# Kernel optimization log

Hardware: AMD Instinct MI355X
Metric: run time of the kernel (lower is better)

Reference implementation:

```python
import jax, jax.numpy as jnp
import numpy as np

N = 100000      # nodes
E = 1600000     # edges
G = 256         # graphs
NF = 2          # dataset.num_features
NC = 2          # dataset.num_classes
DIM = 32
BN_EPS = 1e-5


def _gin_layer(h, src, dst, w_in, b_in, w_out, b_out, gamma, beta):
    # GINConv (eps=0): h' = MLP(h + sum_{j in N(i)} h_j)
    agg = jax.ops.segment_sum(h[src], dst, num_segments=N)  # [N, d] scatter-add
    z = h + agg
    z = jax.nn.relu(z @ w_in + b_in) @ w_out + b_out        # 2-layer MLP
    z = jax.nn.relu(z)
    # BatchNorm1d (training-mode batch stats, biased var as in torch)
    mean = jnp.mean(z, axis=0)
    var = jnp.var(z, axis=0)
    return gamma * (z - mean) * jax.lax.rsqrt(var + BN_EPS) + beta


def setup_inputs() -> dict:
    key = jax.random.key(0)
    ks = jax.random.split(key, 20)
    s = 0.1
    x = jax.random.normal(ks[0], (N, NF), dtype=jnp.float32)
    edge_index = jax.random.randint(ks[1], (2, E), 0, N, dtype=jnp.int64)
    batch = jnp.sort(jax.random.randint(ks[2], (N,), 0, G, dtype=jnp.int64))
    return {
        "x": x,
        "edge_index": edge_index,
        "batch": batch,
        "w1_in": jax.random.normal(ks[3], (NF, DIM), dtype=jnp.float32) * s,
        "b1_in": jnp.zeros((DIM,), jnp.float32),
        "w1_out": jax.random.normal(ks[4], (DIM, DIM), dtype=jnp.float32) * s,
        "b1_out": jnp.zeros((DIM,), jnp.float32),
        "ws_in": jax.random.normal(ks[5], (4, DIM, DIM), dtype=jnp.float32) * s,
        "bs_in": jnp.zeros((4, DIM), jnp.float32),
        "ws_out": jax.random.normal(ks[6], (4, DIM, DIM), dtype=jnp.float32) * s,
        "bs_out": jnp.zeros((4, DIM), jnp.float32),
        "bn_gamma": jnp.ones((5, DIM), jnp.float32),
        "bn_beta": jnp.zeros((5, DIM), jnp.float32),
        "fc1_w": jax.random.normal(ks[7], (DIM, DIM), dtype=jnp.float32) * s,
        "fc1_b": jnp.zeros((DIM,), jnp.float32),
        "fc2_w": jax.random.normal(ks[8], (DIM, NC), dtype=jnp.float32) * s,
        "fc2_b": jnp.zeros((NC,), jnp.float32),
    }


def reference(x, edge_index, batch, w1_in, b1_in, w1_out, b1_out,
              ws_in, bs_in, ws_out, bs_out, bn_gamma, bn_beta,
              fc1_w, fc1_b, fc2_w, fc2_b):
    src, dst = edge_index[0], edge_index[1]
    h = _gin_layer(x, src, dst, w1_in, b1_in, w1_out, b1_out, bn_gamma[0], bn_beta[0])
    for i in range(4):  # convs 2..5 (structurally identical)
        h = _gin_layer(h, src, dst, ws_in[i], bs_in[i], ws_out[i], bs_out[i],
                       bn_gamma[i + 1], bn_beta[i + 1])
    g = jax.ops.segment_sum(h, batch, num_segments=G)  # global_add_pool -> [G, DIM]
    g = jax.nn.relu(g @ fc1_w + fc1_b)
    # dropout is identity in eval mode
    g = g @ fc2_w + fc2_b
    return jax.nn.log_softmax(g, axis=-1)
```

## Files before the change

kernel.cpp:

```cpp
#include <hip/hip_runtime.h>
#include <math.h>

#define NN 100000
#define NE 1600000
#define NG 256
#define NPART 200
#define PS 500
#define CAP 9000
#define EPB 2048
#define NBLK ((NE + EPB - 1) / EPB)
#define DEGB 64
static constexpr float BN_EPS = 1e-5f;

__device__ inline float h2f(unsigned short u) {
    _Float16 h; __builtin_memcpy(&h, &u, 2); return (float)h;
}
__device__ inline unsigned short f2h(float f) {
    _Float16 h = (_Float16)f; unsigned short u; __builtin_memcpy(&u, &h, 2); return u;
}
__device__ inline unsigned int pack2(float a, float b) {
    return (unsigned int)f2h(a) | ((unsigned int)f2h(b) << 16);
}

__global__ __launch_bounds__(256) void bucket_k(const int* __restrict__ src,
                                                const int* __restrict__ dst,
                                                int* __restrict__ bcur,
                                                unsigned int* __restrict__ bpk) {
    __shared__ int cnt[NPART];
    __shared__ int base[NPART];
    int t = threadIdx.x;
    for (int i = t; i < NPART; i += 256) cnt[i] = 0;
    __syncthreads();
    int eb = blockIdx.x * EPB + t * 8;
    bool act = eb < NE;
    int myp[8], myr[8];
    unsigned int pk[8];
    if (act) {
        int4 d0 = *reinterpret_cast<const int4*>(dst + eb);
        int4 d1 = *reinterpret_cast<const int4*>(dst + eb + 4);
        int4 s0 = *reinterpret_cast<const int4*>(src + eb);
        int4 s1 = *reinterpret_cast<const int4*>(src + eb + 4);
        int dd[8] = {d0.x,d0.y,d0.z,d0.w,d1.x,d1.y,d1.z,d1.w};
        int ss[8] = {s0.x,s0.y,s0.z,s0.w,s1.x,s1.y,s1.z,s1.w};
        #pragma unroll
        for (int i = 0; i < 8; i++) {
            int p = dd[i] / PS;
            myp[i] = p;
            pk[i] = ((unsigned int)ss[i] << 9) | (unsigned int)(dd[i] - p * PS);
            myr[i] = atomicAdd(&cnt[p], 1);
        }
    }
    __syncthreads();
    for (int i = t; i < NPART; i += 256)
        base[i] = cnt[i] ? atomicAdd(&bcur[i], cnt[i]) : 0;
    __syncthreads();
    if (act) {
        #pragma unroll
        for (int i = 0; i < 8; i++)
            bpk[myp[i] * CAP + base[myp[i]] + myr[i]] = pk[i];
    }
}

__global__ __launch_bounds__(256) void build_k(const int* __restrict__ bcur,
                                               const unsigned int* __restrict__ bpk,
                                               int* __restrict__ rowptr,
                                               int* __restrict__ csr,
                                               int* __restrict__ perm) {
    __shared__ int hist[PS];
    __shared__ int allc[NPART];
    __shared__ int psum[256];
    __shared__ int bc[DEGB];
    int p = blockIdx.x, t = threadIdx.x;
    int lo = p * PS;
    if (t < NPART) allc[t] = bcur[t];
    for (int i = t; i < PS; i += 256) hist[i] = 0;
    if (t < DEGB) bc[t] = 0;
    __syncthreads();
    int base = 0;
    for (int q = 0; q < p; q++) base += allc[q];
    int cnt = allc[p];
    const unsigned int* bp = bpk + p * CAP;
    const uint4* bp4 = reinterpret_cast<const uint4*>(bp);
    int n4 = cnt >> 2;
    for (int i = t; i < n4; i += 256) {
        uint4 v = bp4[i];
        atomicAdd(&hist[v.x & 511u], 1);
        atomicAdd(&hist[v.y & 511u], 1);
        atomicAdd(&hist[v.z & 511u], 1);
        atomicAdd(&hist[v.w & 511u], 1);
    }
    for (int i = 4 * n4 + t; i < cnt; i += 256) atomicAdd(&hist[bp[i] & 511u], 1);
    __syncthreads();
    int j0 = t * 2;
    int d0v = 0, d1v = 0, tsum = 0;
    if (j0 < PS) {
        d0v = hist[j0]; d1v = hist[j0 + 1];
        tsum = d0v + d1v;
        atomicAdd(&bc[d0v < DEGB ? d0v : DEGB - 1], 1);
        atomicAdd(&bc[d1v < DEGB ? d1v : DEGB - 1], 1);
    }
    psum[t] = tsum;
    __syncthreads();
    for (int off = 1; off < 256; off <<= 1) {
        int v = (t >= off) ? psum[t - off] : 0;
        __syncthreads();
        psum[t] += v;
        __syncthreads();
    }
    int texcl = psum[t] - tsum;
    if (j0 < PS) {
        int run = base + texcl;
        hist[j0] = run; rowptr[lo + j0] = run; run += d0v;
        hist[j0 + 1] = run; rowptr[lo + j0 + 1] = run; run += d1v;
    }
    if (p == NPART - 1 && t == 0) rowptr[NN] = base + cnt;
    __syncthreads();
    if (t == 0) {
        int run = 0;
        #pragma unroll
        for (int b = 0; b < DEGB; b++) { int c = bc[b]; bc[b] = run; run += c; }
    }
    __syncthreads();
    if (j0 < PS) {
        int r0 = atomicAdd(&bc[d0v < DEGB ? d0v : DEGB - 1], 1);
        perm[(PS - 1 - r0) * NPART + p] = lo + j0;
        int r1 = atomicAdd(&bc[d1v < DEGB ? d1v : DEGB - 1], 1);
        perm[(PS - 1 - r1) * NPART + p] = lo + j0 + 1;
    }
    __syncthreads();
    for (int i = t; i < n4; i += 256) {
        uint4 v = bp4[i];
        csr[atomicAdd(&hist[v.x & 511u], 1)] = v.x >> 9;
        csr[atomicAdd(&hist[v.y & 511u], 1)] = v.y >> 9;
        csr[atomicAdd(&hist[v.z & 511u], 1)] = v.z >> 9;
        csr[atomicAdd(&hist[v.w & 511u], 1)] = v.w >> 9;
    }
    for (int i = 4 * n4 + t; i < cnt; i += 256)
        csr[atomicAdd(&hist[bp[i] & 511u], 1)] = bp[i] >> 9;
}

__global__ __launch_bounds__(128) void gmlp1_k(
        const float* __restrict__ x, const int* __restrict__ perm,
        const int* __restrict__ rowptr, const int* __restrict__ csr,
        const float* __restrict__ w_in, const float* __restrict__ b_in,
        const float* __restrict__ w_out, const float* __restrict__ b_out,
        unsigned short* __restrict__ zout, float* __restrict__ stats) {
    __shared__ float lwi[64], lbi[32], lwo[1024], lbo[32];
    __shared__ float zin[64][33];
    int t = threadIdx.x;
    int n = t >> 1, q = t & 1, c0 = q * 16;
    for (int i = t; i < 1024; i += 128) lwo[i] = w_out[i];
    if (t < 64) lwi[t] = w_in[t];
    if (t < 32) { lbi[t] = b_in[t]; lbo[t] = b_out[t]; }
    __syncthreads();
    int gid = blockIdx.x * 64 + n;
    bool act = gid < NN;
    int node = act ? perm[gid] : 0;
    float h0 = 0.f, h1 = 0.f;
    if (act) {
        int rs = rowptr[node], re = rowptr[node + 1];
        if (q == 0) {
            float2 self = *reinterpret_cast<const float2*>(x + 2 * (size_t)node);
            h0 = self.x; h1 = self.y;
        }
        float g0 = 0.f, g1 = 0.f;
        int k = rs + q;
        for (; k + 6 < re; k += 8) {
            int s0 = csr[k], s1 = csr[k + 2], s2 = csr[k + 4], s3 = csr[k + 6];
            float2 v0 = *reinterpret_cast<const float2*>(x + 2 * (size_t)s0);
            float2 v1 = *reinterpret_cast<const float2*>(x + 2 * (size_t)s1);
            float2 v2 = *reinterpret_cast<const float2*>(x + 2 * (size_t)s2);
            float2 v3 = *reinterpret_cast<const float2*>(x + 2 * (size_t)s3);
            h0 += v0.x + v2.x; h1 += v0.y + v2.y;
            g0 += v1.x + v3.x; g1 += v1.y + v3.y;
        }
        for (; k < re; k += 2) {
            int s = csr[k];
            float2 v = *reinterpret_cast<const float2*>(x + 2 * (size_t)s);
            h0 += v.x; h1 += v.y;
        }
        h0 += g0; h1 += g1;
    }
    h0 += __shfl_xor(h0, 1);
    h1 += __shfl_xor(h1, 1);
    float y[16];
    #pragma unroll
    for (int j = 0; j < 16; j++) {
        float a = lbi[c0 + j] + h0 * lwi[c0 + j] + h1 * lwi[32 + c0 + j];
        y[j] = a > 0.f ? a : 0.f;
    }
    #pragma unroll
    for (int j = 0; j < 16; j++) zin[n][c0 + j] = act ? y[j] : 0.f;
    __syncthreads();
    float o[16];
    #pragma unroll
    for (int j = 0; j < 16; j++) o[j] = lbo[c0 + j];
    #pragma unroll
    for (int c = 0; c < 32; c++) {
        float yv = zin[n][c];
        #pragma unroll
        for (int j = 0; j < 16; j++) o[j] += yv * lwo[c * 32 + c0 + j];
    }
    #pragma unroll
    for (int j = 0; j < 16; j++) o[j] = o[j] > 0.f ? o[j] : 0.f;
    if (act) {
        unsigned short* zo = zout + (size_t)node * 32 + c0;
        uint4 wa, wb;
        wa.x = pack2(o[0], o[1]);   wa.y = pack2(o[2], o[3]);
        wa.z = pack2(o[4], o[5]);   wa.w = pack2(o[6], o[7]);
        wb.x = pack2(o[8], o[9]);   wb.y = pack2(o[10], o[11]);
        wb.z = pack2(o[12], o[13]); wb.w = pack2(o[14], o[15]);
        *reinterpret_cast<uint4*>(zo) = wa;
        *reinterpret_cast<uint4*>(zo + 8) = wb;
    }
    __syncthreads();
    #pragma unroll
    for (int j = 0; j < 16; j++) zin[n][c0 + j] = act ? o[j] : 0.f;
    __syncthreads();
    if (t < 32) {
        float s = 0.f, sq = 0.f;
        for (int nn = 0; nn < 64; nn++) {
            float v = zin[nn][t];
            s += v; sq += v * v;
        }
        atomicAdd(&stats[t], s);
        atomicAdd(&stats[32 + t], sq);
    }
}

__global__ __launch_bounds__(128) void gmlp32_k(
        const unsigned short* __restrict__ z, const int* __restrict__ perm,
        const float* __restrict__ statsIn,
        const float* __restrict__ gamma, const float* __restrict__ beta,
        const int* __restrict__ rowptr, const int* __restrict__ csr,
        const float* __restrict__ w_in, const float* __restrict__ b_in,
        const float* __restrict__ w_out, const float* __restrict__ b_out,
        unsigned short* __restrict__ zout, float* __restrict__ statsOut) {
    __shared__ float lwi[1024], lwo[1024], lbi[32], lbo[32], lsc[64];
    __shared__ float zin[64][33];
    int t = threadIdx.x;
    int n = t >> 1, q = t & 1, c0 = q * 16;
    for (int i = t; i < 1024; i += 128) { lwi[i] = w_in[i]; lwo[i] = w_out[i]; }
    if (t < 32) {
        lbi[t] = b_in[t]; lbo[t] = b_out[t];
        float mean = statsIn[t] * (1.f / NN);
        float var  = statsIn[32 + t] * (1.f / NN) - mean * mean;
        float scale = gamma[t] * rsqrtf(var + BN_EPS);
        lsc[t] = scale;
        lsc[32 + t] = beta[t] - mean * scale;
    }
    __syncthreads();
    int gid = blockIdx.x * 64 + n;
    bool act = gid < NN;
    int node = act ? perm[gid] : 0;
    float a[16];
    #pragma unroll
    for (int j = 0; j < 16; j++) a[j] = 0.f;
    float cntf = 0.f;
    if (act) {
        int rs = rowptr[node], re = rowptr[node + 1];
        cntf = (float)(re - rs + 1);
        const unsigned short* zb = z + (size_t)node * 32 + c0;
        uint4 sa = *reinterpret_cast<const uint4*>(zb);
        uint4 sb = *reinterpret_cast<const uint4*>(zb + 8);
        const unsigned short* pa = reinterpret_cast<const unsigned short*>(&sa);
        const unsigned short* pb = reinterpret_cast<const unsigned short*>(&sb);
        #pragma unroll
        for (int j = 0; j < 8; j++) { a[j] = h2f(pa[j]); a[8 + j] = h2f(pb[j]); }
        int k = rs;
        for (; k + 4 <= re; k += 4) {
            int s0 = csr[k], s1 = csr[k + 1], s2 = csr[k + 2], s3 = csr[k + 3];
            const unsigned short* r0 = z + (size_t)s0 * 32 + c0;
            const unsigned short* r1 = z + (size_t)s1 * 32 + c0;
            const unsigned short* r2 = z + (size_t)s2 * 32 + c0;
            const unsigned short* r3 = z + (size_t)s3 * 32 + c0;
            uint4 v0a = *reinterpret_cast<const uint4*>(r0);
            uint4 v0b = *reinterpret_cast<const uint4*>(r0 + 8);
            uint4 v1a = *reinterpret_cast<const uint4*>(r1);
            uint4 v1b = *reinterpret_cast<const uint4*>(r1 + 8);
            uint4 v2a = *reinterpret_cast<const uint4*>(r2);
            uint4 v2b = *reinterpret_cast<const uint4*>(r2 + 8);
            uint4 v3a = *reinterpret_cast<const uint4*>(r3);
            uint4 v3b = *reinterpret_cast<const uint4*>(r3 + 8);
            const unsigned short* q0a = reinterpret_cast<const unsigned short*>(&v0a);
            const unsigned short* q0b = reinterpret_cast<const unsigned short*>(&v0b);
            const unsigned short* q1a = reinterpret_cast<const unsigned short*>(&v1a);
            const unsigned short* q1b = reinterpret_cast<const unsigned short*>(&v1b);
            const unsigned short* q2a = reinterpret_cast<const unsigned short*>(&v2a);
            const unsigned short* q2b = reinterpret_cast<const unsigned short*>(&v2b);
            const unsigned short* q3a = reinterpret_cast<const unsigned short*>(&v3a);
            const unsigned short* q3b = reinterpret_cast<const unsigned short*>(&v3b);
            #pragma unroll
            for (int j = 0; j < 8; j++) {
                a[j]     += (h2f(q0a[j]) + h2f(q1a[j])) + (h2f(q2a[j]) + h2f(q3a[j]));
                a[8 + j] += (h2f(q0b[j]) + h2f(q1b[j])) + (h2f(q2b[j]) + h2f(q3b[j]));
            }
        }
        for (; k < re; k++) {
            int s = csr[k];
            const unsigned short* r = z + (size_t)s * 32 + c0;
            uint4 va = *reinterpret_cast<const uint4*>(r);
            uint4 vb = *reinterpret_cast<const uint4*>(r + 8);
            const unsigned short* qa = reinterpret_cast<const unsigned short*>(&va);
            const unsigned short* qb = reinterpret_cast<const unsigned short*>(&vb);
            #pragma unroll
            for (int j = 0; j < 8; j++) { a[j] += h2f(qa[j]); a[8 + j] += h2f(qb[j]); }
        }
    }
    #pragma unroll
    for (int j = 0; j < 16; j++)
        zin[n][c0 + j] = act ? (a[j] * lsc[c0 + j] + cntf * lsc[32 + c0 + j]) : 0.f;
    __syncthreads();
    float y[16];
    #pragma unroll
    for (int j = 0; j < 16; j++) y[j] = lbi[c0 + j];
    #pragma unroll
    for (int c = 0; c < 32; c++) {
        float zv = zin[n][c];
        #pragma unroll
        for (int j = 0; j < 16; j++) y[j] += zv * lwi[c * 32 + c0 + j];
    }
    #pragma unroll
    for (int j = 0; j < 16; j++) y[j] = y[j] > 0.f ? y[j] : 0.f;
    __syncthreads();
    #pragma unroll
    for (int j = 0; j < 16; j++) zin[n][c0 + j] = y[j];
    __syncthreads();
    float o[16];
    #pragma unroll
    for (int j = 0; j < 16; j++) o[j] = lbo[c0 + j];
    #pragma unroll
    for (int c = 0; c < 32; c++) {
        float yv = zin[n][c];
        #pragma unroll
        for (int j = 0; j < 16; j++) o[j] += yv * lwo[c * 32 + c0 + j];
    }
    #pragma unroll
    for (int j = 0; j < 16; j++) o[j] = o[j] > 0.f ? o[j] : 0.f;
    if (act) {
        unsigned short* zo = zout + (size_t)node * 32 + c0;
        uint4 wa, wb;
        wa.x = pack2(o[0], o[1]);   wa.y = pack2(o[2], o[3]);
        wa.z = pack2(o[4], o[5]);   wa.w = pack2(o[6], o[7]);
        wb.x = pack2(o[8], o[9]);   wb.y = pack2(o[10], o[11]);
        wb.z = pack2(o[12], o[13]); wb.w = pack2(o[14], o[15]);
        *reinterpret_cast<uint4*>(zo) = wa;
        *reinterpret_cast<uint4*>(zo + 8) = wb;
    }
    __syncthreads();
    #pragma unroll
    for (int j = 0; j < 16; j++) zin[n][c0 + j] = act ? o[j] : 0.f;
    __syncthreads();
    if (t < 32) {
        float s = 0.f, sq = 0.f;
        for (int nn = 0; nn < 64; nn++) {
            float v = zin[nn][t];
            s += v; sq += v * v;
        }
        atomicAdd(&statsOut[t], s);
        atomicAdd(&statsOut[32 + t], sq);
    }
}

__global__ __launch_bounds__(256) void pool_seg_k(
        const unsigned short* __restrict__ z,
        const float* __restrict__ statsIn,
        const float* __restrict__ gamma, const float* __restrict__ beta,
        const int* __restrict__ batch, float* __restrict__ g) {
    __shared__ float lsc[64];
    __shared__ float part[32][33];
    int t = threadIdx.x, slot = t >> 3, q = t & 7, c0 = q * 4;
    int gr = blockIdx.x;
    if (t < 32) {
        float mean = statsIn[t] * (1.f / NN);
        float var  = statsIn[32 + t] * (1.f / NN) - mean * mean;
        float scale = gamma[t] * rsqrtf(var + BN_EPS);
        lsc[t] = scale;
        lsc[32 + t] = beta[t] - mean * scale;
    }
    int lo = 0, hi = NN;
    while (lo < hi) { int mid = (lo + hi) >> 1; if (batch[mid] < gr) lo = mid + 1; else hi = mid; }
    int start = lo;
    hi = NN;
    while (lo < hi) { int mid = (lo + hi) >> 1; if (batch[mid] < gr + 1) lo = mid + 1; else hi = mid; }
    int end = lo;
    float a0 = 0.f, a1 = 0.f, a2 = 0.f, a3 = 0.f;
    for (int i = start + slot; i < end; i += 32) {
        ushort4 v = *reinterpret_cast<const ushort4*>(z + (size_t)i * 32 + c0);
        a0 += h2f(v.x); a1 += h2f(v.y); a2 += h2f(v.z); a3 += h2f(v.w);
    }
    part[slot][c0+0] = a0; part[slot][c0+1] = a1;
    part[slot][c0+2] = a2; part[slot][c0+3] = a3;
    __syncthreads();
    if (t < 32) {
        float s = 0.f;
        for (int sl = 0; sl < 32; sl++) s += part[sl][t];
        float cnt = (float)(end - start);
        g[(size_t)gr * 32 + t] = s * lsc[t] + cnt * lsc[32 + t];
    }
}

__global__ __launch_bounds__(256) void head_k(
        const float* __restrict__ g,
        const float* __restrict__ fc1w, const float* __restrict__ fc1b,
        const float* __restrict__ fc2w, const float* __restrict__ fc2b,
        float* __restrict__ out) {
    __shared__ float lw1[1024], lb1[32], lw2[64], lb2[2];
    int t = threadIdx.x;
    for (int i = t; i < 1024; i += 256) lw1[i] = fc1w[i];
    if (t < 32) lb1[t] = fc1b[t];
    if (t < 64) lw2[t] = fc2w[t];
    if (t < 2) lb2[t] = fc2b[t];
    __syncthreads();
    float gv[32];
    #pragma unroll
    for (int c = 0; c < 32; c++) gv[c] = g[(size_t)t * 32 + c];
    float o0 = lb2[0], o1 = lb2[1];
    #pragma unroll 4
    for (int k = 0; k < 32; k++) {
        float a = lb1[k];
        #pragma unroll
        for (int c = 0; c < 32; c++) a += gv[c] * lw1[c * 32 + k];
        a = a > 0.f ? a : 0.f;
        o0 += a * lw2[k * 2 + 0];
        o1 += a * lw2[k * 2 + 1];
    }
    float m = fmaxf(o0, o1);
    float lse = m + logf(expf(o0 - m) + expf(o1 - m));
    out[t * 2 + 0] = o0 - lse;
    out[t * 2 + 1] = o1 - lse;
}

extern "C" void kernel_launch(void* const* d_in, const int* in_sizes, int n_in,
                              void* d_out, int out_size, void* d_ws, size_t ws_size,
                              hipStream_t stream) {
    const float* x      = (const float*)d_in[0];
    const int*   ei     = (const int*)d_in[1];
    const int*   src    = ei;
    const int*   dst    = ei + NE;
    const int*   batch  = (const int*)d_in[2];
    const float* w1_in  = (const float*)d_in[3];
    const float* b1_in  = (const float*)d_in[4];
    const float* w1_out = (const float*)d_in[5];
    const float* b1_out = (const float*)d_in[6];
    const float* ws_in  = (const float*)d_in[7];
    const float* bs_in  = (const float*)d_in[8];
    const float* ws_out = (const float*)d_in[9];
    const float* bs_out = (const float*)d_in[10];
    const float* gamma  = (const float*)d_in[11];
    const float* beta   = (const float*)d_in[12];
    const float* fc1w   = (const float*)d_in[13];
    const float* fc1b   = (const float*)d_in[14];
    const float* fc2w   = (const float*)d_in[15];
    const float* fc2b   = (const float*)d_in[16];
    float* out = (float*)d_out;

    unsigned short* bufA = (unsigned short*)d_ws;
    unsigned short* bufB = bufA + (size_t)NN * 32;
    float* stats  = (float*)(bufB + (size_t)NN * 32);
    int*   bcur   = (int*)(stats + 5 * 64);
    float* g      = (float*)(bcur + NPART);
    int*   perm   = (int*)(g + (size_t)NG * 32);
    int*   rowptr = perm + NN;
    int*   csr    = rowptr + NN + 4;
    unsigned int* bpk = (unsigned int*)(csr + NE);

    hipMemsetAsync(stats, 0, (size_t)(5 * 64 + NPART) * sizeof(int), stream);

    bucket_k<<<NBLK, 256, 0, stream>>>(src, dst, bcur, bpk);
    build_k<<<NPART, 256, 0, stream>>>(bcur, bpk, rowptr, csr, perm);

    gmlp1_k<<<(NN + 63) / 64, 128, 0, stream>>>(x, perm, rowptr, csr,
                                                w1_in, b1_in, w1_out, b1_out, bufA, stats);

    const unsigned short* cur = bufA;
    unsigned short* nxt = bufB;
    for (int j = 0; j < 4; j++) {
        gmlp32_k<<<(NN + 63) / 64, 128, 0, stream>>>(cur, perm, stats + j * 64,
                                              gamma + j * 32, beta + j * 32,
                                              rowptr, csr,
                                              ws_in + j * 1024, bs_in + j * 32,
                                              ws_out + j * 1024, bs_out + j * 32,
                                              nxt, stats + (j + 1) * 64);
        unsigned short* tmp = (unsigned short*)cur; cur = nxt; nxt = tmp;
    }

    pool_seg_k<<<NG, 256, 0, stream>>>(cur, stats + 4 * 64,
                                       gamma + 4 * 32, beta + 4 * 32, batch, g);
    head_k<<<1, 256, 0, stream>>>(g, fc1w, fc1b, fc2w, fc2b, out);
}
```

Measured before the change: 477.4 us.

## Shrink CSR partitions, localize degree-sorted perm, enlarge GIN blocks, unroll gather by 8

Node partitions are halved to 250 nodes (400 partitions), so each build thread handles one node and the packed destination offset uses 8 bits. The degree-sorted permutation is now stored contiguously inside each partition instead of interleaved across partitions, which changes which nodes share a block in the aggregation kernels. The GIN MLP kernel moves to 256-thread blocks of 128 nodes, and its neighbor gather is unrolled by 8 to keep more loads in flight. In exchange it uses more registers and shared memory, and the new perm ordering loses the cross-partition degree balancing.

```diff
diff --git a/kernel.cpp b/kernel.cpp
--- a/kernel.cpp
+++ b/kernel.cpp
@@ -4,9 +4,9 @@
 #define NN 100000
 #define NE 1600000
 #define NG 256
-#define NPART 200
-#define PS 500
-#define CAP 9000
+#define NPART 400
+#define PS 250
+#define CAP 4500
 #define EPB 2048
 #define NBLK ((NE + EPB - 1) / EPB)
 #define DEGB 64
@@ -46,7 +46,7 @@
         for (int i = 0; i < 8; i++) {
             int p = dd[i] / PS;
             myp[i] = p;
-            pk[i] = ((unsigned int)ss[i] << 9) | (unsigned int)(dd[i] - p * PS);
+            pk[i] = ((unsigned int)ss[i] << 8) | (unsigned int)(dd[i] - p * PS);
             myr[i] = atomicAdd(&cnt[p], 1);
         }
     }
@@ -72,7 +72,7 @@
     __shared__ int bc[DEGB];
     int p = blockIdx.x, t = threadIdx.x;
     int lo = p * PS;
-    if (t < NPART) allc[t] = bcur[t];
+    for (int i = t; i < NPART; i += 256) allc[i] = bcur[i];
     for (int i = t; i < PS; i += 256) hist[i] = 0;
     if (t < DEGB) bc[t] = 0;
     __syncthreads();
@@ -84,20 +84,18 @@
     int n4 = cnt >> 2;
     for (int i = t; i < n4; i += 256) {
         uint4 v = bp4[i];
-        atomicAdd(&hist[v.x & 511u], 1);
-        atomicAdd(&hist[v.y & 511u], 1);
-        atomicAdd(&hist[v.z & 511u], 1);
-        atomicAdd(&hist[v.w & 511u], 1);
-    }
-    for (int i = 4 * n4 + t; i < cnt; i += 256) atomicAdd(&hist[bp[i] & 511u], 1);
-    __syncthreads();
-    int j0 = t * 2;
-    int d0v = 0, d1v = 0, tsum = 0;
-    if (j0 < PS) {
-        d0v = hist[j0]; d1v = hist[j0 + 1];
-        tsum = d0v + d1v;
-        atomicAdd(&bc[d0v < DEGB ? d0v : DEGB - 1], 1);
-        atomicAdd(&bc[d1v < DEGB ? d1v : DEGB - 1], 1);
+        atomicAdd(&hist[v.x & 255u], 1);
+        atomicAdd(&hist[v.y & 255u], 1);
+        atomicAdd(&hist[v.z & 255u], 1);
+        atomicAdd(&hist[v.w & 255u], 1);
+    }
+    for (int i = 4 * n4 + t; i < cnt; i += 256) atomicAdd(&hist[bp[i] & 255u], 1);
+    __syncthreads();
+    int dv = 0, tsum = 0;
+    if (t < PS) {
+        dv = hist[t];
+        tsum = dv;
+        atomicAdd(&bc[dv < DEGB ? dv : DEGB - 1], 1);
     }
     psum[t] = tsum;
     __syncthreads();
@@ -108,10 +106,10 @@
         __syncthreads();
     }
     int texcl = psum[t] - tsum;
-    if (j0 < PS) {
+    if (t < PS) {
         int run = base + texcl;
-        hist[j0] = run; rowptr[lo + j0] = run; run += d0v;
-        hist[j0 + 1] = run; rowptr[lo + j0 + 1] = run; run += d1v;
+        hist[t] = run;
+        rowptr[lo + t] = run;
     }
     if (p == NPART - 1 && t == 0) rowptr[NN] = base + cnt;
     __syncthreads();
@@ -121,22 +119,20 @@
         for (int b = 0; b < DEGB; b++) { int c = bc[b]; bc[b] = run; run += c; }
     }
     __syncthreads();
-    if (j0 < PS) {
-        int r0 = atomicAdd(&bc[d0v < DEGB ? d0v : DEGB - 1], 1);
-        perm[(PS - 1 - r0) * NPART + p] = lo + j0;
-        int r1 = atomicAdd(&bc[d1v < DEGB ? d1v : DEGB - 1], 1);
-        perm[(PS - 1 - r1) * NPART + p] = lo + j0 + 1;
+    if (t < PS) {
+        int r = atomicAdd(&bc[dv < DEGB ? dv : DEGB - 1], 1);
+        perm[lo + r] = lo + t;
     }
     __syncthreads();
     for (int i = t; i < n4; i += 256) {
         uint4 v = bp4[i];
-        csr[atomicAdd(&hist[v.x & 511u], 1)] = v.x >> 9;
-        csr[atomicAdd(&hist[v.y & 511u], 1)] = v.y >> 9;
-        csr[atomicAdd(&hist[v.z & 511u], 1)] = v.z >> 9;
-        csr[atomicAdd(&hist[v.w & 511u], 1)] = v.w >> 9;
+        csr[atomicAdd(&hist[v.x & 255u], 1)] = v.x >> 8;
+        csr[atomicAdd(&hist[v.y & 255u], 1)] = v.y >> 8;
+        csr[atomicAdd(&hist[v.z & 255u], 1)] = v.z >> 8;
+        csr[atomicAdd(&hist[v.w & 255u], 1)] = v.w >> 8;
     }
     for (int i = 4 * n4 + t; i < cnt; i += 256)
-        csr[atomicAdd(&hist[bp[i] & 511u], 1)] = bp[i] >> 9;
+        csr[atomicAdd(&hist[bp[i] & 255u], 1)] = bp[i] >> 8;
 }
 
 __global__ __launch_bounds__(128) void gmlp1_k(
@@ -228,7 +224,7 @@
     }
 }
 
-__global__ __launch_bounds__(128) void gmlp32_k(
+__global__ __launch_bounds__(256) void gmlp32_k(
         const unsigned short* __restrict__ z, const int* __restrict__ perm,
         const float* __restrict__ statsIn,
         const float* __restrict__ gamma, const float* __restrict__ beta,
@@ -237,10 +233,10 @@
         const float* __restrict__ w_out, const float* __restrict__ b_out,
         unsigned short* __restrict__ zout, float* __restrict__ statsOut) {
     __shared__ float lwi[1024], lwo[1024], lbi[32], lbo[32], lsc[64];
-    __shared__ float zin[64][33];
+    __shared__ float zin[128][33];
     int t = threadIdx.x;
     int n = t >> 1, q = t & 1, c0 = q * 16;
-    for (int i = t; i < 1024; i += 128) { lwi[i] = w_in[i]; lwo[i] = w_out[i]; }
+    for (int i = t; i < 1024; i += 256) { lwi[i] = w_in[i]; lwo[i] = w_out[i]; }
     if (t < 32) {
         lbi[t] = b_in[t]; lbo[t] = b_out[t];
         float mean = statsIn[t] * (1.f / NN);
@@ -250,7 +246,7 @@
         lsc[32 + t] = beta[t] - mean * scale;
     }
     __syncthreads();
-    int gid = blockIdx.x * 64 + n;
+    int gid = blockIdx.x * 128 + n;
     bool act = gid < NN;
     int node = act ? perm[gid] : 0;
     float a[16];
@@ -268,39 +264,48 @@
         #pragma unroll
         for (int j = 0; j < 8; j++) { a[j] = h2f(pa[j]); a[8 + j] = h2f(pb[j]); }
         int k = rs;
+        for (; k + 8 <= re; k += 8) {
+            uint4 va[8], vb[8];
+            #pragma unroll
+            for (int r = 0; r < 8; r++) {
+                const unsigned short* rp = z + (size_t)csr[k + r] * 32 + c0;
+                va[r] = *reinterpret_cast<const uint4*>(rp);
+                vb[r] = *reinterpret_cast<const uint4*>(rp + 8);
+            }
+            #pragma unroll
+            for (int r = 0; r < 8; r++) {
+                const unsigned short* qa = reinterpret_cast<const unsigned short*>(&va[r]);
+                const unsigned short* qb = reinterpret_cast<const unsigned short*>(&vb[r]);
+                #pragma unroll
+                for (int j = 0; j < 8; j++) {
+                    a[j]     += h2f(qa[j]);
+                    a[8 + j] += h2f(qb[j]);
+                }
+            }
+        }
         for (; k + 4 <= re; k += 4) {
-            int s0 = csr[k], s1 = csr[k + 1], s2 = csr[k + 2], s3 = csr[k + 3];
-            const unsigned short* r0 = z + (size_t)s0 * 32 + c0;
-            const unsigned short* r1 = z + (size_t)s1 * 32 + c0;
-            const unsigned short* r2 = z + (size_t)s2 * 32 + c0;
-            const unsigned short* r3 = z + (size_t)s3 * 32 + c0;
-            uint4 v0a = *reinterpret_cast<const uint4*>(r0);
-            uint4 v0b = *reinterpret_cast<const uint4*>(r0 + 8);
-            uint4 v1a = *reinterpret_cast<const uint4*>(r1);
-            uint4 v1b = *reinterpret_cast<const uint4*>(r1 + 8);
-            uint4 v2a = *reinterpret_cast<const uint4*>(r2);
-            uint4 v2b = *reinterpret_cast<const uint4*>(r2 + 8);
-            uint4 v3a = *reinterpret_cast<const uint4*>(r3);
-            uint4 v3b = *reinterpret_cast<const uint4*>(r3 + 8);
-            const unsigned short* q0a = reinterpret_cast<const unsigned short*>(&v0a);
-            const unsigned short* q0b = reinterpret_cast<const unsigned short*>(&v0b);
-            const unsigned short* q1a = reinterpret_cast<const unsigned short*>(&v1a);
-            const unsigned short* q1b = reinterpret_cast<const unsigned short*>(&v1b);
-            const unsigned short* q2a = reinterpret_cast<const unsigned short*>(&v2a);
-            const unsigned short* q2b = reinterpret_cast<const unsigned short*>(&v2b);
-            const unsigned short* q3a = reinterpret_cast<const unsigned short*>(&v3a);
-            const unsigned short* q3b = reinterpret_cast<const unsigned short*>(&v3b);
+            uint4 va[4], vb[4];
             #pragma unroll
-            for (int j = 0; j < 8; j++) {
-                a[j]     += (h2f(q0a[j]) + h2f(q1a[j])) + (h2f(q2a[j]) + h2f(q3a[j]));
-                a[8 + j] += (h2f(q0b[j]) + h2f(q1b[j])) + (h2f(q2b[j]) + h2f(q3b[j]));
+            for (int r = 0; r < 4; r++) {
+                const unsigned short* rp = z + (size_t)csr[k + r] * 32 + c0;
+                va[r] = *reinterpret_cast<const uint4*>(rp);
+                vb[r] = *reinterpret_cast<const uint4*>(rp + 8);
             }
+            #pragma unroll
+            for (int r = 0; r < 4; r++) {
+                const unsigned short* qa = reinterpret_cast<const unsigned short*>(&va[r]);
+                const unsigned short* qb = reinterpret_cast<const unsigned short*>(&vb[r]);
+                #pragma unroll
+                for (int j = 0; j < 8; j++) {
+                    a[j]     += h2f(qa[j]);
+                    a[8 + j] += h2f(qb[j]);
+                }
+            }
         }
         for (; k < re; k++) {
-            int s = csr[k];
-            const unsigned short* r = z + (size_t)s * 32 + c0;
-            uint4 va = *reinterpret_cast<const uint4*>(r);
-            uint4 vb = *reinterpret_cast<const uint4*>(r + 8);
+            const unsigned short* rp = z + (size_t)csr[k] * 32 + c0;
+            uint4 va = *reinterpret_cast<const uint4*>(rp);
+            uint4 vb = *reinterpret_cast<const uint4*>(rp + 8);
             const unsigned short* qa = reinterpret_cast<const unsigned short*>(&va);
             const unsigned short* qb = reinterpret_cast<const unsigned short*>(&vb);
             #pragma unroll
@@ -353,7 +358,7 @@
     __syncthreads();
     if (t < 32) {
         float s = 0.f, sq = 0.f;
-        for (int nn = 0; nn < 64; nn++) {
+        for (int nn = 0; nn < 128; nn++) {
             float v = zin[nn][t];
             s += v; sq += v * v;
         }
@@ -476,7 +481,7 @@
     const unsigned short* cur = bufA;
     unsigned short* nxt = bufB;
     for (int j = 0; j < 4; j++) {
-        gmlp32_k<<<(NN + 63) / 64, 128, 0, stream>>>(cur, perm, stats + j * 64,
+        gmlp32_k<<<(NN + 127) / 128, 256, 0, stream>>>(cur, perm, stats + j * 64,
                                               gamma + j * 32, beta + j * 32,
                                               rowptr, csr,
                                               ws_in + j * 1024, bs_in + j * 32,
```

New measurement: 447.9 us. -6.2%, faster.
